# Kernel optimization log

Measured on AMD Instinct MI355X. Metric: run time of the kernel, lower is better.

Reference implementation:

```python
import jax, jax.numpy as jnp
import numpy as np


def setup_inputs() -> dict:
    key = jax.random.key(0)
    k1, k2, k3, k4 = jax.random.split(key, 4)
    B, C, W, H = 4, 64, 512, 512
    cF = jax.random.normal(k1, (B, C, W, H), dtype=jnp.float32)
    sF = jax.random.uniform(k2, (B, C, W, H), dtype=jnp.float32)
    alpha = jnp.array([0.6], dtype=jnp.float32)
    # style eigenvalues: strictly > 1e-5 so k_s == C (full rank), matching the
    # module's k_s = sum(s_e > 1e-5) slicing when the style SVD is well-conditioned
    s_e = jax.random.uniform(k3, (B, C), dtype=jnp.float32) + 0.5
    s_v = jax.random.normal(k4, (B, C, C), dtype=jnp.float32)
    return {"cF": cF, "sF": sF, "alpha": alpha, "s_e": s_e, "s_v": s_v}


def reference(cF, sF, alpha, s_e, s_v):
    B, C, W, H = cF.shape
    N = W * H
    cf = cF.reshape(B, C, N)            # [B, C, WH]
    sf = sF.reshape(B, C, -1)           # [B, C, W1H1]

    # ---- whiten content ----
    c_mean = jnp.mean(cf, axis=2, keepdims=True)
    cfc = cf - c_mean                   # centered content
    # covariance + I  (I shift => all eigenvalues >= 1, so k_c == C)
    cov = jnp.einsum('bcn,bdn->bcd', cfc, cfc) / (N - 1) + jnp.eye(C, dtype=cf.dtype)
    _, c_e, c_vh = jnp.linalg.svd(cov, full_matrices=False)
    c_d = c_e ** -0.5
    # original: step2 = (Vh @ diag(c_d)) @ Vh^T  -> fuse diag as column scale
    step2 = jnp.einsum('bij,bj,blj->bil', c_vh, c_d, c_vh)
    whiten_cF = jnp.einsum('bcd,bdn->bcn', step2, cfc)

    # ---- color with style stats ----
    s_mean = jnp.mean(sf, axis=2, keepdims=True)
    s_d = s_e ** 0.5                    # k_s == C by construction of s_e
    colorM = jnp.einsum('bij,bj,blj->bil', s_v, s_d, s_v)
    target = jnp.einsum('bcd,bdn->bcn', colorM, whiten_cF) + s_mean

    a = alpha.reshape(())
    csF = a * target + (1.0 - a) * cf
    return csF.reshape(B, C, W, H).astype(jnp.float32)
```

## Files before the change

kernel.cpp:

```cpp
#include <hip/hip_runtime.h>
#include <math.h>

#define WS_G 0
#define WS_SC 16384
#define WS_SS 16640
#define WS_T 16896
#define WS_BIAS 33280
#define WS_ZERO_COUNT 16896

typedef __attribute__((ext_vector_type(8))) short bf16x8;
typedef __attribute__((ext_vector_type(16))) float f32x16;

__device__ __forceinline__ float waveRed(float v) {
#pragma unroll
    for (int o = 32; o > 0; o >>= 1) v += __shfl_down(v, o, 64);
    return v;
}

__global__ void zero_kernel(float* __restrict__ ws, int n) {
    int i = blockIdx.x * 256 + threadIdx.x;
    if (i < n) ws[i] = 0.f;
}

#define GR_SLAB 1040
#define GR_PLANE 16640
__global__ __launch_bounds__(256) void pre_kernel(const float* __restrict__ cF,
                                                  const float* __restrict__ sF,
                                                  float* __restrict__ G,
                                                  float* __restrict__ Sc,
                                                  float* __restrict__ Ss, int N) {
    __shared__ __align__(16) char smem[2 * GR_PLANE];
    const int t = threadIdx.x;
    if (blockIdx.x < 2048) {
        const int ch = blockIdx.x >> 3;
        const int part = blockIdx.x & 7;
        const int seg = N >> 3;
        const float4* p = reinterpret_cast<const float4*>(sF + (size_t)ch * N + (size_t)part * seg);
        const int nf4 = seg >> 2;
        float acc = 0.f;
        for (int i = t; i < nf4; i += 256) {
            float4 v = p[i];
            acc += (v.x + v.y) + (v.z + v.w);
        }
        acc = waveRed(acc);
        float* red = reinterpret_cast<float*>(smem);
        if ((t & 63) == 0) red[t >> 6] = acc;
        __syncthreads();
        if (t == 0) atomicAdd(&Ss[ch], (red[0] + red[1]) + (red[2] + red[3]));
        return;
    }
    const int bid2 = blockIdx.x - 2048;
    const int b = bid2 >> 7;
    const int part = bid2 & 127;
    const float* base = cF + (size_t)b * 64 * N + (size_t)part * (N >> 7);
    const int wid = t >> 6;
    const int lane = t & 63;
    const int I = (wid >> 1) << 5;
    const int Jt = (wid & 1) << 5;
    const bool diag = (I == Jt);
    const int rA = I + (lane & 31);
    const int rB = Jt + (lane & 31);
    const int sl = lane >> 5;

    f32x16 acc = {};
    float rs[8];
#pragma unroll
    for (int i = 0; i < 8; ++i) rs[i] = 0.f;

    float4 v[8];
#pragma unroll
    for (int i = 0; i < 8; ++i) {
        int f = t + 256 * i;
        v[i] = *reinterpret_cast<const float4*>(base + (size_t)(f >> 5) * N + (f & 31) * 4);
    }

    for (int c = 0; c < 16; ++c) {
        uint2 hw[8], lw[8];
#pragma unroll
        for (int i = 0; i < 8; ++i) {
            float4 x = v[i];
            rs[i] += (x.x + x.y) + (x.z + x.w);
            unsigned bx = __float_as_uint(x.x), by = __float_as_uint(x.y);
            unsigned bz = __float_as_uint(x.z), bw = __float_as_uint(x.w);
            float lx = x.x - __uint_as_float(bx & 0xffff0000u);
            float ly = x.y - __uint_as_float(by & 0xffff0000u);
            float lz = x.z - __uint_as_float(bz & 0xffff0000u);
            float lwv = x.w - __uint_as_float(bw & 0xffff0000u);
            hw[i] = make_uint2((bx >> 16) | (by & 0xffff0000u),
                               (bz >> 16) | (bw & 0xffff0000u));
            lw[i] = make_uint2((__float_as_uint(lx) >> 16) | (__float_as_uint(ly) & 0xffff0000u),
                               (__float_as_uint(lz) >> 16) | (__float_as_uint(lwv) & 0xffff0000u));
        }
        __syncthreads();
#pragma unroll
        for (int i = 0; i < 8; ++i) {
            int f = t + 256 * i;
            int row = f >> 5, col4 = f & 31;
            char* dst = smem + (col4 >> 1) * GR_SLAB + row * 16 + ((col4 & 1) << 3);
            *reinterpret_cast<uint2*>(dst) = hw[i];
            *reinterpret_cast<uint2*>(dst + GR_PLANE) = lw[i];
        }
        if (c < 15) {
            const float* gn = base + (c + 1) * 128;
#pragma unroll
            for (int i = 0; i < 8; ++i) {
                int f = t + 256 * i;
                v[i] = *reinterpret_cast<const float4*>(gn + (size_t)(f >> 5) * N + (f & 31) * 4);
            }
        }
        __syncthreads();
#pragma unroll
        for (int kc = 0; kc < 8; ++kc) {
            const char* sb = smem + (2 * kc + sl) * GR_SLAB;
            bf16x8 ahi = *reinterpret_cast<const bf16x8*>(sb + rA * 16);
            bf16x8 alo = *reinterpret_cast<const bf16x8*>(sb + GR_PLANE + rA * 16);
            bf16x8 bhi, blo;
            if (diag) {
                bhi = ahi; blo = alo;
            } else {
                bhi = *reinterpret_cast<const bf16x8*>(sb + rB * 16);
                blo = *reinterpret_cast<const bf16x8*>(sb + GR_PLANE + rB * 16);
            }
            acc = __builtin_amdgcn_mfma_f32_32x32x16_bf16(ahi, bhi, acc, 0, 0, 0);
            acc = __builtin_amdgcn_mfma_f32_32x32x16_bf16(ahi, blo, acc, 0, 0, 0);
            acc = __builtin_amdgcn_mfma_f32_32x32x16_bf16(alo, bhi, acc, 0, 0, 0);
        }
        __syncthreads();
    }

    float* Gb = G + b * 4096;
#pragma unroll
    for (int r = 0; r < 16; ++r) {
        int m = (r & 3) + 8 * (r >> 2) + 4 * (lane >> 5);
        int n = lane & 31;
        atomicAdd(&Gb[(I + m) * 64 + (Jt + n)], acc[r]);
    }
    const int baseRow = t >> 5;
#pragma unroll
    for (int i = 0; i < 8; ++i) {
        float s = rs[i];
#pragma unroll
        for (int o = 16; o > 0; o >>= 1) s += __shfl_xor(s, o);
        if ((lane & 31) == 0) atomicAdd(&Sc[b * 64 + baseRow + 8 * i], s);
    }
}

#define SSTR 68

__device__ __forceinline__ void matmul44(float* __restrict__ D, const float* __restrict__ A,
                                         const float* __restrict__ Bm, int i0, int j0) {
    float acc[4][4];
#pragma unroll
    for (int i = 0; i < 4; ++i)
#pragma unroll
        for (int j = 0; j < 4; ++j) acc[i][j] = 0.f;
    for (int k = 0; k < 64; ++k) {
        float4 bv = *reinterpret_cast<const float4*>(&Bm[k * SSTR + j0]);
        float a0 = A[(i0 + 0) * SSTR + k];
        float a1 = A[(i0 + 1) * SSTR + k];
        float a2 = A[(i0 + 2) * SSTR + k];
        float a3 = A[(i0 + 3) * SSTR + k];
        acc[0][0] += a0 * bv.x; acc[0][1] += a0 * bv.y; acc[0][2] += a0 * bv.z; acc[0][3] += a0 * bv.w;
        acc[1][0] += a1 * bv.x; acc[1][1] += a1 * bv.y; acc[1][2] += a1 * bv.z; acc[1][3] += a1 * bv.w;
        acc[2][0] += a2 * bv.x; acc[2][1] += a2 * bv.y; acc[2][2] += a2 * bv.z; acc[2][3] += a2 * bv.w;
        acc[3][0] += a3 * bv.x; acc[3][1] += a3 * bv.y; acc[3][2] += a3 * bv.z; acc[3][3] += a3 * bv.w;
    }
#pragma unroll
    for (int i = 0; i < 4; ++i)
#pragma unroll
        for (int j = 0; j < 4; ++j) D[(i0 + i) * SSTR + j0 + j] = acc[i][j];
}

__global__ __launch_bounds__(256) void solve_kernel(const float* __restrict__ G,
                                                    const float* __restrict__ Sc,
                                                    const float* __restrict__ Ss,
                                                    const float* __restrict__ alphap,
                                                    const float* __restrict__ s_e,
                                                    const float* __restrict__ s_v,
                                                    float* __restrict__ Tg,
                                                    float* __restrict__ biasg, int N) {
    __shared__ __align__(16) float Abuf[64 * SSTR];
    __shared__ __align__(16) float Ybuf[64 * SSTR];
    __shared__ __align__(16) float Tbuf[64 * SSTR];
    __shared__ __align__(16) float Wb[64 * 20];
    __shared__ float sdv[64], mcv[64], msv[64];
    __shared__ float redv;
    const int b = blockIdx.x, t = threadIdx.x;
    const int i0 = (t >> 4) << 2, j0 = (t & 15) << 2;
    const float invN = 1.f / (float)N;
    const float invNm1 = 1.f / (float)(N - 1);
    if (t < 64) {
        mcv[t] = Sc[b * 64 + t] * invN;
        msv[t] = Ss[b * 64 + t] * invN;
        sdv[t] = sqrtf(s_e[b * 64 + t]);
    }
    __syncthreads();
#pragma unroll
    for (int i = 0; i < 4; ++i) {
        float mi = mcv[i0 + i];
#pragma unroll
        for (int j = 0; j < 4; ++j) {
            float g = G[b * 4096 + (i0 + i) * 64 + j0 + j];
            float cov = (g - mi * mcv[j0 + j] * (float)N) * invNm1 + (((i0 + i) == (j0 + j)) ? 1.f : 0.f);
            Abuf[(i0 + i) * SSTR + j0 + j] = cov;
        }
    }
    __syncthreads();
    if (t < 64) {
        float d = waveRed(Abuf[t * SSTR + t]);
        if (t == 0) redv = d * (1.f / 64.f);
    }
    __syncthreads();
    const float s = redv;
    const float inv_s = 1.f / s;
#pragma unroll
    for (int i = 0; i < 4; ++i)
#pragma unroll
        for (int j = 0; j < 4; ++j) {
            Abuf[(i0 + i) * SSTR + j0 + j] *= inv_s;
            Ybuf[(i0 + i) * SSTR + j0 + j] = ((i0 + i) == (j0 + j)) ? 1.f : 0.f;
        }
    __syncthreads();
    const int kr = t >> 2;
    const int cw = (t & 3) << 2;
    for (int it = 0; it < 3; ++it) {
        matmul44(Tbuf, Ybuf, Ybuf, i0, j0);
        __syncthreads();
        for (int lb = 0; lb < 4; ++lb) {
            const int cb = lb << 4;
            float w0 = 0.f, w1 = 0.f, w2 = 0.f, w3 = 0.f;
            for (int j = 0; j < 64; ++j) {
                float a = Abuf[kr * SSTR + j];
                float4 tv = *reinterpret_cast<const float4*>(&Tbuf[j * SSTR + cb + cw]);
                w0 += a * tv.x; w1 += a * tv.y; w2 += a * tv.z; w3 += a * tv.w;
            }
            Wb[kr * 20 + cw + 0] = ((kr == cb + cw + 0) ? 1.5f : 0.f) - 0.5f * w0;
            Wb[kr * 20 + cw + 1] = ((kr == cb + cw + 1) ? 1.5f : 0.f) - 0.5f * w1;
            Wb[kr * 20 + cw + 2] = ((kr == cb + cw + 2) ? 1.5f : 0.f) - 0.5f * w2;
            Wb[kr * 20 + cw + 3] = ((kr == cb + cw + 3) ? 1.5f : 0.f) - 0.5f * w3;
            __syncthreads();
            float y0 = 0.f, y1 = 0.f, y2 = 0.f, y3 = 0.f;
            for (int k = 0; k < 64; ++k) {
                float a = Ybuf[kr * SSTR + k];
                float4 wv = *reinterpret_cast<const float4*>(&Wb[k * 20 + cw]);
                y0 += a * wv.x; y1 += a * wv.y; y2 += a * wv.z; y3 += a * wv.w;
            }
            Tbuf[kr * SSTR + cb + cw + 0] = y0;
            Tbuf[kr * SSTR + cb + cw + 1] = y1;
            Tbuf[kr * SSTR + cb + cw + 2] = y2;
            Tbuf[kr * SSTR + cb + cw + 3] = y3;
            __syncthreads();
        }
#pragma unroll
        for (int i = 0; i < 4; ++i)
#pragma unroll
            for (int j = 0; j < 4; ++j)
                Ybuf[(i0 + i) * SSTR + j0 + j] = Tbuf[(i0 + i) * SSTR + j0 + j];
        __syncthreads();
    }
    for (int i = 0; i < 16; ++i) {
        int idx = t + 256 * i;
        Abuf[(idx >> 6) * SSTR + (idx & 63)] = s_v[b * 4096 + idx];
    }
    __syncthreads();
    {
        float acc[4][4];
#pragma unroll
        for (int i = 0; i < 4; ++i)
#pragma unroll
            for (int j = 0; j < 4; ++j) acc[i][j] = 0.f;
        for (int k = 0; k < 64; ++k) {
            float sd = sdv[k];
            float a0 = Abuf[(i0 + 0) * SSTR + k] * sd;
            float a1 = Abuf[(i0 + 1) * SSTR + k] * sd;
            float a2 = Abuf[(i0 + 2) * SSTR + k] * sd;
            float a3 = Abuf[(i0 + 3) * SSTR + k] * sd;
            float c0v = Abuf[(j0 + 0) * SSTR + k];
            float c1v = Abuf[(j0 + 1) * SSTR + k];
            float c2v = Abuf[(j0 + 2) * SSTR + k];
            float c3v = Abuf[(j0 + 3) * SSTR + k];
            acc[0][0] += a0 * c0v; acc[0][1] += a0 * c1v; acc[0][2] += a0 * c2v; acc[0][3] += a0 * c3v;
            acc[1][0] += a1 * c0v; acc[1][1] += a1 * c1v; acc[1][2] += a1 * c2v; acc[1][3] += a1 * c3v;
            acc[2][0] += a2 * c0v; acc[2][1] += a2 * c1v; acc[2][2] += a2 * c2v; acc[2][3] += a2 * c3v;
            acc[3][0] += a3 * c0v; acc[3][1] += a3 * c1v; acc[3][2] += a3 * c2v; acc[3][3] += a3 * c3v;
        }
        __syncthreads();
#pragma unroll
        for (int i = 0; i < 4; ++i)
#pragma unroll
            for (int j = 0; j < 4; ++j) Tbuf[(i0 + i) * SSTR + j0 + j] = acc[i][j];
    }
    __syncthreads();
    matmul44(Abuf, Tbuf, Ybuf, i0, j0);
    __syncthreads();
    const float alpha_v = alphap[0];
    const float fac = alpha_v / sqrtf(s);
#pragma unroll
    for (int i = 0; i < 4; ++i)
#pragma unroll
        for (int j = 0; j < 4; ++j) {
            float m = Abuf[(i0 + i) * SSTR + j0 + j] * fac;
            if ((i0 + i) == (j0 + j)) m += 1.f - alpha_v;
            Tg[b * 4096 + (i0 + i) * 64 + j0 + j] = m;
        }
    if (t < 64) {
        float acc = 0.f;
        for (int d = 0; d < 64; ++d) acc += Abuf[t * SSTR + d] * mcv[d];
        biasg[b * 64 + t] = alpha_v * msv[t] - fac * acc;
    }
}

#define APX 128
#define XSTR 72
__global__ __launch_bounds__(256) void apply_kernel(const float* __restrict__ cF,
                                                    const float* __restrict__ Tg,
                                                    const float* __restrict__ biasg,
                                                    float* __restrict__ out, int N) {
    __shared__ __align__(16) unsigned short sx[2][APX][XSTR];
    __shared__ float bl[64];
    const int b = blockIdx.x >> 11;
    const int part = blockIdx.x & 2047;
    const float* src = cF + (size_t)b * 64 * N + (size_t)part * APX;
    float* dst = out + (size_t)b * 64 * N + (size_t)part * APX;
    const int t = threadIdx.x;
    const int lane = t & 63;
    const int wid = t >> 6;
    if (t < 64) bl[t] = biasg[b * 64 + t];

    const int I = (wid & 1) << 5;
    const int xb0 = (wid >> 1) << 6;
    const int kb = (lane >> 5) << 3;
    bf16x8 th[4], tl[4];
    {
        const float* Trow = Tg + b * 4096 + (size_t)(I + (lane & 31)) * 64;
#pragma unroll
        for (int ks = 0; ks < 4; ++ks) {
            float4 u0 = *reinterpret_cast<const float4*>(Trow + ks * 16 + kb);
            float4 u1 = *reinterpret_cast<const float4*>(Trow + ks * 16 + kb + 4);
            float v[8] = {u0.x, u0.y, u0.z, u0.w, u1.x, u1.y, u1.z, u1.w};
#pragma unroll
            for (int j = 0; j < 8; ++j) {
                unsigned u = __float_as_uint(v[j]);
                th[ks][j] = (short)(u >> 16);
                float r = v[j] - __uint_as_float(u & 0xffff0000u);
                tl[ks][j] = (short)(__float_as_uint(r) >> 16);
            }
        }
    }

#pragma unroll
    for (int i = 0; i < 4; ++i) {
        int u = t + 256 * i;
        int kp = u >> 5;
        int x0 = (u & 31) << 2;
        const float* ra = src + (size_t)(2 * kp) * N + x0;
        float4 va = *reinterpret_cast<const float4*>(ra);
        float4 vb = *reinterpret_cast<const float4*>(ra + N);
        float av[4] = {va.x, va.y, va.z, va.w};
        float bv[4] = {vb.x, vb.y, vb.z, vb.w};
#pragma unroll
        for (int j = 0; j < 4; ++j) {
            unsigned ua = __float_as_uint(av[j]);
            unsigned ub = __float_as_uint(bv[j]);
            float ral = av[j] - __uint_as_float(ua & 0xffff0000u);
            float rbl = bv[j] - __uint_as_float(ub & 0xffff0000u);
            unsigned hi = (ua >> 16) | (ub & 0xffff0000u);
            unsigned lo = (__float_as_uint(ral) >> 16) | (__float_as_uint(rbl) & 0xffff0000u);
            *reinterpret_cast<unsigned*>(&sx[0][x0 + j][2 * kp]) = hi;
            *reinterpret_cast<unsigned*>(&sx[1][x0 + j][2 * kp]) = lo;
        }
    }
    __syncthreads();

    f32x16 acc0 = {}, acc1 = {};
    const int xA = xb0 + (lane & 31);
#pragma unroll
    for (int ks = 0; ks < 4; ++ks) {
        const int ko = ks * 16 + kb;
        bf16x8 bh0 = *reinterpret_cast<const bf16x8*>(&sx[0][xA][ko]);
        bf16x8 bL0 = *reinterpret_cast<const bf16x8*>(&sx[1][xA][ko]);
        bf16x8 bh1 = *reinterpret_cast<const bf16x8*>(&sx[0][xA + 32][ko]);
        bf16x8 bL1 = *reinterpret_cast<const bf16x8*>(&sx[1][xA + 32][ko]);
        acc0 = __builtin_amdgcn_mfma_f32_32x32x16_bf16(th[ks], bh0, acc0, 0, 0, 0);
        acc0 = __builtin_amdgcn_mfma_f32_32x32x16_bf16(th[ks], bL0, acc0, 0, 0, 0);
        acc0 = __builtin_amdgcn_mfma_f32_32x32x16_bf16(tl[ks], bh0, acc0, 0, 0, 0);
        acc1 = __builtin_amdgcn_mfma_f32_32x32x16_bf16(th[ks], bh1, acc1, 0, 0, 0);
        acc1 = __builtin_amdgcn_mfma_f32_32x32x16_bf16(th[ks], bL1, acc1, 0, 0, 0);
        acc1 = __builtin_amdgcn_mfma_f32_32x32x16_bf16(tl[ks], bh1, acc1, 0, 0, 0);
    }

#pragma unroll
    for (int r = 0; r < 16; ++r) {
        int m = (r & 3) + 8 * (r >> 2) + 4 * (lane >> 5);
        float bb = bl[I + m];
        float* dr = dst + (size_t)(I + m) * N;
        dr[xA] = acc0[r] + bb;
        dr[xA + 32] = acc1[r] + bb;
    }
}

extern "C" void kernel_launch(void* const* d_in, const int* in_sizes, int n_in,
                              void* d_out, int out_size, void* d_ws, size_t ws_size,
                              hipStream_t stream) {
    const float* cF = (const float*)d_in[0];
    const float* sF = (const float*)d_in[1];
    const float* alpha = (const float*)d_in[2];
    const float* s_e = (const float*)d_in[3];
    const float* s_v = (const float*)d_in[4];
    float* out = (float*)d_out;
    float* ws = (float*)d_ws;
    const int B = 4, C = 64;
    const int N = in_sizes[0] / (B * C);
    float* G = ws + WS_G;
    float* Sc = ws + WS_SC;
    float* Ss = ws + WS_SS;
    float* T = ws + WS_T;
    float* bias = ws + WS_BIAS;
    hipLaunchKernelGGL(zero_kernel, dim3(66), dim3(256), 0, stream, ws, WS_ZERO_COUNT);
    hipLaunchKernelGGL(pre_kernel, dim3(2048 + B * 128), dim3(256), 0, stream, cF, sF, G, Sc, Ss, N);
    hipLaunchKernelGGL(solve_kernel, dim3(B), dim3(256), 0, stream, G, Sc, Ss, alpha, s_e, s_v, T, bias, N);
    hipLaunchKernelGGL(apply_kernel, dim3(B * 2048), dim3(256), 0, stream, cF, T, bias, out, N);
}
```

Before: 737.2 us.

## Split style-sum from Gram kernel, double-buffer Gram loads, restructure apply loads

```diff
diff --git a/kernel.cpp b/kernel.cpp
--- a/kernel.cpp
+++ b/kernel.cpp
@@ -22,37 +22,86 @@
     if (i < n) ws[i] = 0.f;
 }
 
+__global__ __launch_bounds__(256) void sum_kernel(const float* __restrict__ x,
+                                                  float* __restrict__ sums, int N) {
+    const int ch = blockIdx.x >> 3;
+    const int part = blockIdx.x & 7;
+    const int seg = N >> 3;
+    const float4* p = reinterpret_cast<const float4*>(x + (size_t)ch * N + (size_t)part * seg);
+    const int nf4 = seg >> 2;
+    float a0 = 0.f, a1 = 0.f, a2 = 0.f, a3 = 0.f;
+    for (int i = threadIdx.x; i < nf4; i += 1024) {
+        float4 v0 = p[i];
+        float4 v1 = p[i + 256];
+        float4 v2 = p[i + 512];
+        float4 v3 = p[i + 768];
+        a0 += (v0.x + v0.y) + (v0.z + v0.w);
+        a1 += (v1.x + v1.y) + (v1.z + v1.w);
+        a2 += (v2.x + v2.y) + (v2.z + v2.w);
+        a3 += (v3.x + v3.y) + (v3.z + v3.w);
+    }
+    float acc = waveRed((a0 + a1) + (a2 + a3));
+    __shared__ float red[4];
+    if ((threadIdx.x & 63) == 0) red[threadIdx.x >> 6] = acc;
+    __syncthreads();
+    if (threadIdx.x == 0) atomicAdd(&sums[ch], (red[0] + red[1]) + (red[2] + red[3]));
+}
+
 #define GR_SLAB 1040
 #define GR_PLANE 16640
-__global__ __launch_bounds__(256) void pre_kernel(const float* __restrict__ cF,
-                                                  const float* __restrict__ sF,
-                                                  float* __restrict__ G,
-                                                  float* __restrict__ Sc,
-                                                  float* __restrict__ Ss, int N) {
+
+#define GR_LOAD(dst, cofs)                                                          \
+    _Pragma("unroll") for (int i = 0; i < 8; ++i) {                                 \
+        int f = t + 256 * i;                                                        \
+        dst[i] = *reinterpret_cast<const float4*>(base + (size_t)(cofs) * 128 +     \
+                                                  (size_t)(f >> 5) * N + (f & 31) * 4); \
+    }
+
+#define GR_CONVWRITE(srcv)                                                          \
+    _Pragma("unroll") for (int i = 0; i < 8; ++i) {                                 \
+        float4 x = srcv[i];                                                         \
+        rs[i] += (x.x + x.y) + (x.z + x.w);                                         \
+        unsigned bx = __float_as_uint(x.x), by = __float_as_uint(x.y);              \
+        unsigned bz = __float_as_uint(x.z), bw = __float_as_uint(x.w);              \
+        float lx = x.x - __uint_as_float(bx & 0xffff0000u);                         \
+        float ly = x.y - __uint_as_float(by & 0xffff0000u);                         \
+        float lz = x.z - __uint_as_float(bz & 0xffff0000u);                         \
+        float lwv = x.w - __uint_as_float(bw & 0xffff0000u);                        \
+        uint2 hwv = make_uint2((bx >> 16) | (by & 0xffff0000u),                     \
+                               (bz >> 16) | (bw & 0xffff0000u));                    \
+        uint2 lwv2 = make_uint2((__float_as_uint(lx) >> 16) | (__float_as_uint(ly) & 0xffff0000u), \
+                                (__float_as_uint(lz) >> 16) | (__float_as_uint(lwv) & 0xffff0000u)); \
+        int f = t + 256 * i;                                                        \
+        int row = f >> 5, col4 = f & 31;                                            \
+        char* dstp = smem + (col4 >> 1) * GR_SLAB + row * 16 + ((col4 & 1) << 3);   \
+        *reinterpret_cast<uint2*>(dstp) = hwv;                                      \
+        *reinterpret_cast<uint2*>(dstp + GR_PLANE) = lwv2;                          \
+    }
+
+#define GR_MFMA()                                                                   \
+    _Pragma("unroll") for (int kc = 0; kc < 8; ++kc) {                              \
+        const char* sb = smem + (2 * kc + sl) * GR_SLAB;                            \
+        bf16x8 ahi = *reinterpret_cast<const bf16x8*>(sb + rA * 16);                \
+        bf16x8 alo = *reinterpret_cast<const bf16x8*>(sb + GR_PLANE + rA * 16);     \
+        bf16x8 bhi, blo;                                                            \
+        if (diag) { bhi = ahi; blo = alo; }                                         \
+        else {                                                                      \
+            bhi = *reinterpret_cast<const bf16x8*>(sb + rB * 16);                   \
+            blo = *reinterpret_cast<const bf16x8*>(sb + GR_PLANE + rB * 16);        \
+        }                                                                           \
+        acc = __builtin_amdgcn_mfma_f32_32x32x16_bf16(ahi, bhi, acc, 0, 0, 0);      \
+        acc = __builtin_amdgcn_mfma_f32_32x32x16_bf16(ahi, blo, acc, 0, 0, 0);      \
+        acc = __builtin_amdgcn_mfma_f32_32x32x16_bf16(alo, bhi, acc, 0, 0, 0);      \
+    }
+
+__global__ __launch_bounds__(256) void gram_kernel(const float* __restrict__ cF,
+                                                   float* __restrict__ G,
+                                                   float* __restrict__ Sc, int N) {
     __shared__ __align__(16) char smem[2 * GR_PLANE];
+    const int b = blockIdx.x >> 7;
+    const int part = blockIdx.x & 127;
+    const float* base = cF + (size_t)b * 64 * N + (size_t)part * (N >> 7);
     const int t = threadIdx.x;
-    if (blockIdx.x < 2048) {
-        const int ch = blockIdx.x >> 3;
-        const int part = blockIdx.x & 7;
-        const int seg = N >> 3;
-        const float4* p = reinterpret_cast<const float4*>(sF + (size_t)ch * N + (size_t)part * seg);
-        const int nf4 = seg >> 2;
-        float acc = 0.f;
-        for (int i = t; i < nf4; i += 256) {
-            float4 v = p[i];
-            acc += (v.x + v.y) + (v.z + v.w);
-        }
-        acc = waveRed(acc);
-        float* red = reinterpret_cast<float*>(smem);
-        if ((t & 63) == 0) red[t >> 6] = acc;
-        __syncthreads();
-        if (t == 0) atomicAdd(&Ss[ch], (red[0] + red[1]) + (red[2] + red[3]));
-        return;
-    }
-    const int bid2 = blockIdx.x - 2048;
-    const int b = bid2 >> 7;
-    const int part = bid2 & 127;
-    const float* base = cF + (size_t)b * 64 * N + (size_t)part * (N >> 7);
     const int wid = t >> 6;
     const int lane = t & 63;
     const int I = (wid >> 1) << 5;
@@ -67,65 +116,20 @@
 #pragma unroll
     for (int i = 0; i < 8; ++i) rs[i] = 0.f;
 
-    float4 v[8];
-#pragma unroll
-    for (int i = 0; i < 8; ++i) {
-        int f = t + 256 * i;
-        v[i] = *reinterpret_cast<const float4*>(base + (size_t)(f >> 5) * N + (f & 31) * 4);
-    }
-
-    for (int c = 0; c < 16; ++c) {
-        uint2 hw[8], lw[8];
-#pragma unroll
-        for (int i = 0; i < 8; ++i) {
-            float4 x = v[i];
-            rs[i] += (x.x + x.y) + (x.z + x.w);
-            unsigned bx = __float_as_uint(x.x), by = __float_as_uint(x.y);
-            unsigned bz = __float_as_uint(x.z), bw = __float_as_uint(x.w);
-            float lx = x.x - __uint_as_float(bx & 0xffff0000u);
-            float ly = x.y - __uint_as_float(by & 0xffff0000u);
-            float lz = x.z - __uint_as_float(bz & 0xffff0000u);
-            float lwv = x.w - __uint_as_float(bw & 0xffff0000u);
-            hw[i] = make_uint2((bx >> 16) | (by & 0xffff0000u),
-                               (bz >> 16) | (bw & 0xffff0000u));
-            lw[i] = make_uint2((__float_as_uint(lx) >> 16) | (__float_as_uint(ly) & 0xffff0000u),
-                               (__float_as_uint(lz) >> 16) | (__float_as_uint(lwv) & 0xffff0000u));
-        }
-        __syncthreads();
-#pragma unroll
-        for (int i = 0; i < 8; ++i) {
-            int f = t + 256 * i;
-            int row = f >> 5, col4 = f & 31;
-            char* dst = smem + (col4 >> 1) * GR_SLAB + row * 16 + ((col4 & 1) << 3);
-            *reinterpret_cast<uint2*>(dst) = hw[i];
-            *reinterpret_cast<uint2*>(dst + GR_PLANE) = lw[i];
-        }
-        if (c < 15) {
-            const float* gn = base + (c + 1) * 128;
-#pragma unroll
-            for (int i = 0; i < 8; ++i) {
-                int f = t + 256 * i;
-                v[i] = *reinterpret_cast<const float4*>(gn + (size_t)(f >> 5) * N + (f & 31) * 4);
-            }
-        }
-        __syncthreads();
-#pragma unroll
-        for (int kc = 0; kc < 8; ++kc) {
-            const char* sb = smem + (2 * kc + sl) * GR_SLAB;
-            bf16x8 ahi = *reinterpret_cast<const bf16x8*>(sb + rA * 16);
-            bf16x8 alo = *reinterpret_cast<const bf16x8*>(sb + GR_PLANE + rA * 16);
-            bf16x8 bhi, blo;
-            if (diag) {
-                bhi = ahi; blo = alo;
-            } else {
-                bhi = *reinterpret_cast<const bf16x8*>(sb + rB * 16);
-                blo = *reinterpret_cast<const bf16x8*>(sb + GR_PLANE + rB * 16);
-            }
-            acc = __builtin_amdgcn_mfma_f32_32x32x16_bf16(ahi, bhi, acc, 0, 0, 0);
-            acc = __builtin_amdgcn_mfma_f32_32x32x16_bf16(ahi, blo, acc, 0, 0, 0);
-            acc = __builtin_amdgcn_mfma_f32_32x32x16_bf16(alo, bhi, acc, 0, 0, 0);
-        }
-        __syncthreads();
+    float4 va[8], vb[8];
+    GR_LOAD(va, 0)
+
+    for (int c = 0; c < 16; c += 2) {
+        if (c + 1 < 16) { GR_LOAD(vb, c + 1) }
+        __syncthreads();
+        GR_CONVWRITE(va)
+        __syncthreads();
+        GR_MFMA()
+        if (c + 2 < 16) { GR_LOAD(va, c + 2) }
+        __syncthreads();
+        GR_CONVWRITE(vb)
+        __syncthreads();
+        GR_MFMA()
     }
 
     float* Gb = G + b * 4096;
@@ -325,6 +329,14 @@
     const int t = threadIdx.x;
     const int lane = t & 63;
     const int wid = t >> 6;
+
+    const int p2 = t & 63;
+    const int koct = (t >> 6) << 4;
+    float2 vv[16];
+#pragma unroll
+    for (int j = 0; j < 16; ++j)
+        vv[j] = *reinterpret_cast<const float2*>(src + (size_t)(koct + j) * N + 2 * p2);
+
     if (t < 64) bl[t] = biasg[b * 64 + t];
 
     const int I = (wid & 1) << 5;
@@ -349,25 +361,29 @@
     }
 
 #pragma unroll
-    for (int i = 0; i < 4; ++i) {
-        int u = t + 256 * i;
-        int kp = u >> 5;
-        int x0 = (u & 31) << 2;
-        const float* ra = src + (size_t)(2 * kp) * N + x0;
-        float4 va = *reinterpret_cast<const float4*>(ra);
-        float4 vb = *reinterpret_cast<const float4*>(ra + N);
-        float av[4] = {va.x, va.y, va.z, va.w};
-        float bv[4] = {vb.x, vb.y, vb.z, vb.w};
-#pragma unroll
-        for (int j = 0; j < 4; ++j) {
-            unsigned ua = __float_as_uint(av[j]);
-            unsigned ub = __float_as_uint(bv[j]);
-            float ral = av[j] - __uint_as_float(ua & 0xffff0000u);
-            float rbl = bv[j] - __uint_as_float(ub & 0xffff0000u);
-            unsigned hi = (ua >> 16) | (ub & 0xffff0000u);
-            unsigned lo = (__float_as_uint(ral) >> 16) | (__float_as_uint(rbl) & 0xffff0000u);
-            *reinterpret_cast<unsigned*>(&sx[0][x0 + j][2 * kp]) = hi;
-            *reinterpret_cast<unsigned*>(&sx[1][x0 + j][2 * kp]) = lo;
+    for (int xx = 0; xx < 2; ++xx) {
+#pragma unroll
+        for (int ch = 0; ch < 2; ++ch) {
+            unsigned h0, h1, h2, h3, l0, l1, l2, l3;
+#define CONV_PAIR(jp, HO, LO)                                                     \
+            {                                                                     \
+                float a = xx ? vv[ch * 8 + 2 * jp].y : vv[ch * 8 + 2 * jp].x;     \
+                float bq = xx ? vv[ch * 8 + 2 * jp + 1].y : vv[ch * 8 + 2 * jp + 1].x; \
+                unsigned ua = __float_as_uint(a), ub = __float_as_uint(bq);       \
+                float ra = a - __uint_as_float(ua & 0xffff0000u);                 \
+                float rb = bq - __uint_as_float(ub & 0xffff0000u);                \
+                HO = (ua >> 16) | (ub & 0xffff0000u);                             \
+                LO = (__float_as_uint(ra) >> 16) | (__float_as_uint(rb) & 0xffff0000u); \
+            }
+            CONV_PAIR(0, h0, l0)
+            CONV_PAIR(1, h1, l1)
+            CONV_PAIR(2, h2, l2)
+            CONV_PAIR(3, h3, l3)
+#undef CONV_PAIR
+            uint4 H; H.x = h0; H.y = h1; H.z = h2; H.w = h3;
+            uint4 L; L.x = l0; L.y = l1; L.z = l2; L.w = l3;
+            *reinterpret_cast<uint4*>(&sx[0][2 * p2 + xx][koct + ch * 8]) = H;
+            *reinterpret_cast<uint4*>(&sx[1][2 * p2 + xx][koct + ch * 8]) = L;
         }
     }
     __syncthreads();
@@ -417,7 +433,8 @@
     float* T = ws + WS_T;
     float* bias = ws + WS_BIAS;
     hipLaunchKernelGGL(zero_kernel, dim3(66), dim3(256), 0, stream, ws, WS_ZERO_COUNT);
-    hipLaunchKernelGGL(pre_kernel, dim3(2048 + B * 128), dim3(256), 0, stream, cF, sF, G, Sc, Ss, N);
+    hipLaunchKernelGGL(sum_kernel, dim3(B * C * 8), dim3(256), 0, stream, sF, Ss, N);
+    hipLaunchKernelGGL(gram_kernel, dim3(B * 128), dim3(256), 0, stream, cF, G, Sc, N);
     hipLaunchKernelGGL(solve_kernel, dim3(B), dim3(256), 0, stream, G, Sc, Ss, alpha, s_e, s_v, T, bias, N);
     hipLaunchKernelGGL(apply_kernel, dim3(B * 2048), dim3(256), 0, stream, cF, T, bias, out, N);
 }
```

After: 727.2 us. No clear change (-1.4%).
